# Performance work log

Measured on AMD Instinct MI355X. Metric: run time of the kernel, lower is better.

## Reference

```python
import jax, jax.numpy as jnp
import numpy as np

N = 50000
E = 800000
IN_CH, HID, OUT_CH = 8, 64, 1
NEG_SLOPE = 0.2


def setup_inputs() -> dict:
    key = jax.random.key(0)
    ks = jax.random.split(key, 16)
    x = jax.random.normal(ks[0], (N, IN_CH), dtype=jnp.float32)
    edge_index = jax.random.randint(ks[1], (2, E), 0, N, dtype=jnp.int64)
    def glorot(k, shape):
        fan = shape[0] + shape[-1]
        return jax.random.uniform(k, shape, jnp.float32, -1.0, 1.0) * jnp.sqrt(6.0 / fan)
    # layer 1: in=8 -> 4 heads x 64, concat=False (mean over heads)
    W1 = glorot(ks[2], (IN_CH, 4 * HID))
    as1 = glorot(ks[3], (4, HID)); ad1 = glorot(ks[4], (4, HID))
    b1 = jnp.zeros((HID,), jnp.float32)
    # layer 2: 64 -> 4 heads x 64
    W2 = glorot(ks[5], (HID, 4 * HID))
    as2 = glorot(ks[6], (4, HID)); ad2 = glorot(ks[7], (4, HID))
    b2 = jnp.zeros((HID,), jnp.float32)
    # layer 3: 64 -> 1 head x 1
    W3 = glorot(ks[8], (HID, OUT_CH))
    as3 = glorot(ks[9], (1, OUT_CH)); ad3 = glorot(ks[10], (1, OUT_CH))
    b3 = jnp.zeros((OUT_CH,), jnp.float32)
    return {"x": x, "edge_index": edge_index,
            "W1": W1, "b1": b1, "as1": as1, "ad1": ad1,
            "W2": W2, "b2": b2, "as2": as2, "ad2": ad2,
            "W3": W3, "b3": b3, "as3": as3, "ad3": ad3}


def gat_conv(x, src, dst, W, b, a_src, a_dst, n_nodes):
    """PyG GATConv, concat=False (mean over heads), add_self_loops already applied."""
    heads, ch = a_src.shape
    h = (x @ W).reshape(n_nodes, heads, ch)            # [N,H,C]
    e_src = jnp.sum(h * a_src[None], axis=-1)          # [N,H]
    e_dst = jnp.sum(h * a_dst[None], axis=-1)          # [N,H]
    logits = jax.nn.leaky_relu(e_src[src] + e_dst[dst], NEG_SLOPE)  # [E,H]
    # softmax over incoming edges of each destination node (self loops ensure non-empty)
    m = jax.ops.segment_max(logits, dst, num_segments=n_nodes)      # [N,H]
    ex = jnp.exp(logits - m[dst])
    denom = jax.ops.segment_sum(ex, dst, num_segments=n_nodes)      # [N,H]
    alpha = ex / (denom[dst] + 1e-16)                  # [E,H]
    out = jax.ops.segment_sum(alpha[:, :, None] * h[src], dst, num_segments=n_nodes)  # [N,H,C]
    return jnp.mean(out, axis=1) + b                   # [N,C]


def reference(x, edge_index, W1, b1, as1, ad1, W2, b2, as2, ad2, W3, b3, as3, ad3):
    n = x.shape[0]
    loops = jnp.arange(n, dtype=edge_index.dtype)
    src = jnp.concatenate([edge_index[0], loops])
    dst = jnp.concatenate([edge_index[1], loops])
    h = jax.nn.elu(gat_conv(x, src, dst, W1, b1, as1, ad1, n))
    # Dropout(p=0.2) is identity in eval mode
    h = jax.nn.elu(gat_conv(h, src, dst, W2, b2, as2, ad2, n))
    out = jax.nn.sigmoid(gat_conv(h, src, dst, W3, b3, as3, ad3, n))
    return out  # [N,1] failure probability per node
```

## Files before the change

kernel.cpp:

```cpp
#include <hip/hip_runtime.h>
#include <hip/hip_bf16.h>
#include <hip/hip_fp16.h>
#include <math.h>

#define N_NODES 50000
#define N_EDGES 800000
#define N_TOT   (N_EDGES + N_NODES)
#define NEG_SLOPE 0.2f

static __device__ __forceinline__ float lrelu(float x){ return x >= 0.f ? x : NEG_SLOPE * x; }

__global__ void k_init(const int* __restrict__ ei, int* __restrict__ flag,
                       int* __restrict__ deg){
  int i = blockIdx.x * blockDim.x + threadIdx.x;
  if (i == 0){
    int o = 0;
    #pragma unroll
    for (int j = 1; j < 16; j += 2) o |= ei[j];
    *flag = (o == 0) ? 1 : 0;
  }
  if (i < N_NODES) deg[i] = 1;
}

__global__ void k_count(const int* __restrict__ ei, const int* __restrict__ flag,
                        int* __restrict__ deg){
  int t = blockIdx.x * blockDim.x + threadIdx.x;
  if (t >= N_EDGES / 4) return;
  int d0, d1, d2, d3;
  if (*flag){
    int4 a = *(const int4*)&ei[2 * N_EDGES + 8 * t];
    int4 b = *(const int4*)&ei[2 * N_EDGES + 8 * t + 4];
    d0 = a.x; d1 = a.z; d2 = b.x; d3 = b.z;
  } else {
    int4 a = *(const int4*)&ei[N_EDGES + 4 * t];
    d0 = a.x; d1 = a.y; d2 = a.z; d3 = a.w;
  }
  atomicAdd(&deg[d0], 1);
  atomicAdd(&deg[d1], 1);
  atomicAdd(&deg[d2], 1);
  atomicAdd(&deg[d3], 1);
}

__global__ void k_scan1(const int* __restrict__ deg, int* __restrict__ rowptr,
                        int* __restrict__ bsum){
  __shared__ int sd[256];
  int t = threadIdx.x;
  int base = blockIdx.x * 1024 + t * 4;
  int v0 = (base + 0 < N_NODES) ? deg[base + 0] : 0;
  int v1 = (base + 1 < N_NODES) ? deg[base + 1] : 0;
  int v2 = (base + 2 < N_NODES) ? deg[base + 2] : 0;
  int v3 = (base + 3 < N_NODES) ? deg[base + 3] : 0;
  int tsum = v0 + v1 + v2 + v3;
  sd[t] = tsum; __syncthreads();
  for (int off = 1; off < 256; off <<= 1){
    int vv = (t >= off) ? sd[t - off] : 0;
    __syncthreads();
    sd[t] += vv;
    __syncthreads();
  }
  int excl = sd[t] - tsum;
  if (base + 0 < N_NODES) rowptr[base + 0] = excl;
  if (base + 1 < N_NODES) rowptr[base + 1] = excl + v0;
  if (base + 2 < N_NODES) rowptr[base + 2] = excl + v0 + v1;
  if (base + 3 < N_NODES) rowptr[base + 3] = excl + v0 + v1 + v2;
  if (t == 255) bsum[blockIdx.x] = sd[255];
}

#define NB_SCAN 49
__global__ void k_scan3(int* __restrict__ rowptr, const int* __restrict__ bsum,
                        int* __restrict__ fill){
  __shared__ int sboff[64];
  int t = threadIdx.x;
  if (t < 64){
    int v = (t < NB_SCAN) ? bsum[t] : 0;
    int incl = v;
    #pragma unroll
    for (int off = 1; off < 64; off <<= 1){
      int u = __shfl_up(incl, off);
      if (t >= off) incl += u;
    }
    sboff[t] = incl - v;
  }
  __syncthreads();
  int i = blockIdx.x * blockDim.x + t;
  if (i < N_NODES){
    int v = rowptr[i] + sboff[i >> 10];
    rowptr[i] = v;
    fill[i] = v;
  }
  if (i == 0) rowptr[N_NODES] = N_TOT;
}

__global__ void k_scatter(const int* __restrict__ ei, const int* __restrict__ flag,
                          int* __restrict__ fill, int* __restrict__ col){
  int t = blockIdx.x * blockDim.x + threadIdx.x;
  if (t < N_EDGES / 4){
    int s0, s1, s2, s3, d0, d1, d2, d3;
    if (*flag){
      int4 sa = *(const int4*)&ei[8 * t];
      int4 sb = *(const int4*)&ei[8 * t + 4];
      int4 da = *(const int4*)&ei[2 * N_EDGES + 8 * t];
      int4 db = *(const int4*)&ei[2 * N_EDGES + 8 * t + 4];
      s0 = sa.x; s1 = sa.z; s2 = sb.x; s3 = sb.z;
      d0 = da.x; d1 = da.z; d2 = db.x; d3 = db.z;
    } else {
      int4 sa = *(const int4*)&ei[4 * t];
      int4 da = *(const int4*)&ei[N_EDGES + 4 * t];
      s0 = sa.x; s1 = sa.y; s2 = sa.z; s3 = sa.w;
      d0 = da.x; d1 = da.y; d2 = da.z; d3 = da.w;
    }
    col[atomicAdd(&fill[d0], 1)] = s0;
    col[atomicAdd(&fill[d1], 1)] = s1;
    col[atomicAdd(&fill[d2], 1)] = s2;
    col[atomicAdd(&fill[d3], 1)] = s3;
  } else {
    int n = t - N_EDGES / 4;
    if (n < N_NODES) col[atomicAdd(&fill[n], 1)] = n;
  }
}


__global__ __launch_bounds__(256) void k_transform1(
    const float* __restrict__ xin, const float* __restrict__ W,
    const float* __restrict__ aS, const float* __restrict__ aD,
    __half* __restrict__ h, float* __restrict__ es, float* __restrict__ ed){
  __shared__ float wl[8 * 256];
  int tid = threadIdx.x;
  for (int i = tid; i < 8 * 256; i += 256) wl[i] = W[i];
  int lane = tid & 63, wv = tid >> 6, head = lane >> 4;
  float4 s4 = *(const float4*)&aS[4 * lane];
  float4 d4 = *(const float4*)&aD[4 * lane];
  __syncthreads();
  int base = (blockIdx.x * 4 + wv) * 8;
  for (int m = 0; m < 8; m++){
    int n = base + m;
    if (n >= N_NODES) break;
    float4 xa = *(const float4*)&xin[n * 8];
    float4 xb = *(const float4*)&xin[n * 8 + 4];
    float xs0 = xa.x, xs1 = xa.y, xs2 = xa.z, xs3 = xa.w;
    float xs4 = xb.x, xs5 = xb.y, xs6 = xb.z, xs7 = xb.w;
    float4 acc = make_float4(0.f, 0.f, 0.f, 0.f);
    #define T1STEP(k, xv) { float4 w4 = *(const float4*)&wl[(k)*256 + 4*lane]; \
      acc.x = fmaf(xv, w4.x, acc.x); acc.y = fmaf(xv, w4.y, acc.y); \
      acc.z = fmaf(xv, w4.z, acc.z); acc.w = fmaf(xv, w4.w, acc.w); }
    T1STEP(0, xs0) T1STEP(1, xs1) T1STEP(2, xs2) T1STEP(3, xs3)
    T1STEP(4, xs4) T1STEP(5, xs5) T1STEP(6, xs6) T1STEP(7, xs7)
    #undef T1STEP
    __half2 p0 = __floats2half2_rn(acc.x, acc.y);
    __half2 p1 = __floats2half2_rn(acc.z, acc.w);
    uint2 u; u.x = *(unsigned int*)&p0; u.y = *(unsigned int*)&p1;
    *(uint2*)&h[(size_t)n * 256 + 4 * lane] = u;
    float ps = acc.x*s4.x + acc.y*s4.y + acc.z*s4.z + acc.w*s4.w;
    float pd = acc.x*d4.x + acc.y*d4.y + acc.z*d4.z + acc.w*d4.w;
    #pragma unroll
    for (int off = 1; off < 16; off <<= 1){ ps += __shfl_xor(ps, off); pd += __shfl_xor(pd, off); }
    if ((lane & 15) == 0){ es[n * 4 + head] = ps; ed[n * 4 + head] = pd; }
  }
}

__global__ __launch_bounds__(256) void k_transform2(
    const float* __restrict__ xin, const float* __restrict__ W,
    const float* __restrict__ aS, const float* __restrict__ aD,
    __half* __restrict__ h, float* __restrict__ es, float* __restrict__ ed){
  __shared__ float wl[32 * 256];
  int tid = threadIdx.x;
  int lane = tid & 63, wv = tid >> 6, head = lane >> 4;
  float4 s4 = *(const float4*)&aS[4 * lane];
  float4 d4 = *(const float4*)&aD[4 * lane];
  int base = (blockIdx.x * 4 + wv) * 8;
  float xr[8];
  #pragma unroll
  for (int m = 0; m < 8; m++){
    int n = base + m;
    xr[m] = (n < N_NODES) ? xin[(size_t)n * 64 + lane] : 0.f;
  }
  float4 acc[8];
  #pragma unroll
  for (int m = 0; m < 8; m++) acc[m] = make_float4(0.f, 0.f, 0.f, 0.f);
  for (int hf = 0; hf < 2; hf++){
    if (hf) __syncthreads();
    const float4* Wv = (const float4*)(W + hf * 32 * 256);
    float4* wlv = (float4*)wl;
    #pragma unroll
    for (int i = 0; i < 8; i++) wlv[tid + 256 * i] = Wv[tid + 256 * i];
    __syncthreads();
    #pragma unroll 4
    for (int k = 0; k < 32; k++){
      float4 w4 = *(const float4*)&wl[k * 256 + 4 * lane];
      #pragma unroll
      for (int m = 0; m < 8; m++){
        float xv = __shfl(xr[m], hf * 32 + k);
        acc[m].x = fmaf(xv, w4.x, acc[m].x);
        acc[m].y = fmaf(xv, w4.y, acc[m].y);
        acc[m].z = fmaf(xv, w4.z, acc[m].z);
        acc[m].w = fmaf(xv, w4.w, acc[m].w);
      }
    }
  }
  #pragma unroll
  for (int m = 0; m < 8; m++){
    int n = base + m;
    if (n >= N_NODES) break;
    __half2 p0 = __floats2half2_rn(acc[m].x, acc[m].y);
    __half2 p1 = __floats2half2_rn(acc[m].z, acc[m].w);
    uint2 u; u.x = *(unsigned int*)&p0; u.y = *(unsigned int*)&p1;
    *(uint2*)&h[(size_t)n * 256 + 4 * lane] = u;
    float ps = acc[m].x*s4.x + acc[m].y*s4.y + acc[m].z*s4.z + acc[m].w*s4.w;
    float pd = acc[m].x*d4.x + acc[m].y*d4.y + acc[m].z*d4.z + acc[m].w*d4.w;
    #pragma unroll
    for (int off = 1; off < 16; off <<= 1){ ps += __shfl_xor(ps, off); pd += __shfl_xor(pd, off); }
    if ((lane & 15) == 0){ es[n * 4 + head] = ps; ed[n * 4 + head] = pd; }
  }
}

__global__ __launch_bounds__(256) void k_transform3(
    const float* __restrict__ xin, const float* __restrict__ W3,
    const float* __restrict__ aS, const float* __restrict__ aD,
    float2* __restrict__ pk, float* __restrict__ ed3){
  int gid = blockIdx.x * blockDim.x + threadIdx.x;
  int n = gid >> 6, lane = gid & 63;
  if (n >= N_NODES) return;
  float v = xin[(size_t)n * 64 + lane] * W3[lane];
  #pragma unroll
  for (int off = 1; off < 64; off <<= 1) v += __shfl_xor(v, off);
  if (lane == 0){
    pk[n] = make_float2(v * aS[0], v);
    ed3[n] = v * aD[0];
  }
}

static __device__ __forceinline__ void agg_step(float4& acc, uint2 u, float wt){
  float2 aa = __half22float2(*(__half2*)&u.x);
  float2 bb = __half22float2(*(__half2*)&u.y);
  acc.x = fmaf(wt, aa.x, acc.x); acc.y = fmaf(wt, aa.y, acc.y);
  acc.z = fmaf(wt, bb.x, acc.z); acc.w = fmaf(wt, bb.y, acc.w);
}

__global__ __launch_bounds__(256) void k_agg(
    const __half* __restrict__ h, const float* __restrict__ es, const float* __restrict__ ed,
    const int* __restrict__ rowptr, const int* __restrict__ col,
    const float* __restrict__ bias, float* __restrict__ outf){
  int gid = blockIdx.x * blockDim.x + threadIdx.x;
  int d = gid >> 6, lane = gid & 63;
  if (d >= N_NODES) return;
  int start = rowptr[d], end = rowptr[d + 1];
  int head = lane >> 4;
  float eh = ed[d * 4 + head];
  const __half* hp = h + 4 * lane;
  float4 acc = make_float4(0.f, 0.f, 0.f, 0.f);
  float wsum = 0.f;
  int i = start;
  for (; i + 4 <= end; i += 4){
    int s0 = col[i], s1 = col[i + 1], s2 = col[i + 2], s3 = col[i + 3];
    uint2 u0 = *(const uint2*)(hp + (size_t)s0 * 256);
    uint2 u1 = *(const uint2*)(hp + (size_t)s1 * 256);
    uint2 u2 = *(const uint2*)(hp + (size_t)s2 * 256);
    uint2 u3 = *(const uint2*)(hp + (size_t)s3 * 256);
    float e0 = es[s0 * 4 + head], e1 = es[s1 * 4 + head];
    float e2 = es[s2 * 4 + head], e3 = es[s3 * 4 + head];
    float w0 = __expf(lrelu(e0 + eh));
    float w1 = __expf(lrelu(e1 + eh));
    float w2 = __expf(lrelu(e2 + eh));
    float w3 = __expf(lrelu(e3 + eh));
    wsum += (w0 + w1) + (w2 + w3);
    agg_step(acc, u0, w0); agg_step(acc, u1, w1);
    agg_step(acc, u2, w2); agg_step(acc, u3, w3);
  }
  for (; i < end; i++){
    int s0 = col[i];
    uint2 u0 = *(const uint2*)(hp + (size_t)s0 * 256);
    float w0 = __expf(lrelu(es[s0 * 4 + head] + eh));
    wsum += w0;
    agg_step(acc, u0, w0);
  }
  float inv = 1.0f / (wsum + 1e-16f);
  acc.x *= inv; acc.y *= inv; acc.z *= inv; acc.w *= inv;
  #pragma unroll
  for (int off = 16; off < 64; off <<= 1){
    acc.x += __shfl_xor(acc.x, off);
    acc.y += __shfl_xor(acc.y, off);
    acc.z += __shfl_xor(acc.z, off);
    acc.w += __shfl_xor(acc.w, off);
  }
  if (lane < 16){
    float4 b4 = *(const float4*)&bias[4 * lane];
    float ox = 0.25f * acc.x + b4.x;
    float oy = 0.25f * acc.y + b4.y;
    float oz = 0.25f * acc.z + b4.z;
    float ow = 0.25f * acc.w + b4.w;
    ox = ox > 0.f ? ox : expm1f(ox);
    oy = oy > 0.f ? oy : expm1f(oy);
    oz = oz > 0.f ? oz : expm1f(oz);
    ow = ow > 0.f ? ow : expm1f(ow);
    float4 o = make_float4(ox, oy, oz, ow);
    *(float4*)&outf[(size_t)d * 64 + 4 * lane] = o;
  }
}

__global__ __launch_bounds__(256) void k_agg3(
    const float2* __restrict__ pk, const float* __restrict__ ed3,
    const int* __restrict__ rowptr, const int* __restrict__ col,
    const float* __restrict__ b3, float* __restrict__ out){
  int gid = blockIdx.x * blockDim.x + threadIdx.x;
  int wv = gid >> 6, lane = gid & 63;
  int sub = lane >> 4, li = lane & 15;
  int d = wv * 4 + sub;
  if (d < N_NODES){
    int start = rowptr[d], end = rowptr[d + 1];
    float edv = ed3[d];
    float num = 0.f, den = 0.f;
    for (int i = start + li; i < end; i += 16){
      float2 p = pk[col[i]];
      float wgt = __expf(lrelu(p.x + edv));
      den += wgt;
      num = fmaf(wgt, p.y, num);
    }
    #pragma unroll
    for (int off = 1; off < 16; off <<= 1){
      num += __shfl_xor(num, off);
      den += __shfl_xor(den, off);
    }
    if (li == 0){
      float v = num / (den + 1e-16f) + b3[0];
      out[d] = 1.f / (1.f + __expf(-v));
    }
  }
}

extern "C" void kernel_launch(void* const* d_in, const int* in_sizes, int n_in,
                              void* d_out, int out_size, void* d_ws, size_t ws_size,
                              hipStream_t stream) {
  const float* x   = (const float*)d_in[0];
  const int*   ei  = (const int*)  d_in[1];
  const float* W1  = (const float*)d_in[2];
  const float* b1  = (const float*)d_in[3];
  const float* as1 = (const float*)d_in[4];
  const float* ad1 = (const float*)d_in[5];
  const float* W2  = (const float*)d_in[6];
  const float* b2  = (const float*)d_in[7];
  const float* as2 = (const float*)d_in[8];
  const float* ad2 = (const float*)d_in[9];
  const float* W3  = (const float*)d_in[10];
  const float* b3  = (const float*)d_in[11];
  const float* as3 = (const float*)d_in[12];
  const float* ad3 = (const float*)d_in[13];
  float* out = (float*)d_out;

  char* w = (char*)d_ws;
  size_t off = 0;
  auto alloc = [&](size_t bytes) -> char* {
    char* p = w + off;
    off += (bytes + 255) & ~size_t(255);
    return p;
  };
  int*    flag   = (int*)   alloc(64);
  int*    deg    = (int*)   alloc(N_NODES * 4);
  int*    fill   = (int*)   alloc(N_NODES * 4);
  int*    rowptr = (int*)   alloc((N_NODES + 1) * 4);
  int*    bsum   = (int*)   alloc(64 * 4);
  int*    col    = (int*)   alloc((size_t)N_TOT * 4);
  __half* h      = (__half*)alloc((size_t)N_NODES * 256 * 2);
  float*  es     = (float*) alloc((size_t)N_NODES * 4 * 4);
  float*  ed     = (float*) alloc((size_t)N_NODES * 4 * 4);
  float*  feat1  = (float*) alloc((size_t)N_NODES * 64 * 4);
  float*  feat2  = (float*) alloc((size_t)N_NODES * 64 * 4);
  float2* pk     = (float2*)alloc((size_t)N_NODES * 8);
  float*  ed3    = (float*) alloc(N_NODES * 4);
  (void)ws_size; (void)in_sizes; (void)n_in; (void)out_size;

  k_init   <<<(N_NODES + 255) / 256, 256, 0, stream>>>(ei, flag, deg);
  k_count  <<<(N_EDGES / 4 + 255) / 256, 256, 0, stream>>>(ei, flag, deg);
  k_scan1  <<<NB_SCAN, 256, 0, stream>>>(deg, rowptr, bsum);
  k_scan3  <<<(N_NODES + 255) / 256, 256, 0, stream>>>(rowptr, bsum, fill);
  k_scatter<<<(N_EDGES / 4 + N_NODES + 255) / 256, 256, 0, stream>>>(ei, flag, fill, col);

  const int grid_t12 = (N_NODES + 31) / 32;
  const int grid_wpn = (N_NODES * 64 + 255) / 256;
  const int grid_w4n = ((N_NODES + 3) / 4 * 64 + 255) / 256;

  k_transform1<<<grid_t12, 256, 0, stream>>>(x, W1, as1, ad1, h, es, ed);
  k_agg       <<<grid_wpn, 256, 0, stream>>>(h, es, ed, rowptr, col, b1, feat1);
  k_transform2<<<grid_t12, 256, 0, stream>>>(feat1, W2, as2, ad2, h, es, ed);
  k_agg       <<<grid_wpn, 256, 0, stream>>>(h, es, ed, rowptr, col, b2, feat2);
  k_transform3<<<grid_wpn, 256, 0, stream>>>(feat2, W3, as3, ad3, pk, ed3);
  k_agg3      <<<grid_w4n, 256, 0, stream>>>(pk, ed3, rowptr, col, b3, out);
}
```

Baseline: 394.0 us.

## Fuse CSR count with layer-1 transform and merge scan kernels

Merges degree counting and the layer-1 feature transform into one launch by giving each a separate range of blocks. The two scan passes are collapsed into a single kernel that uses an atomic counter and a spin-wait so each block can read the other blocks' partial sums. The init kernel is replaced by a memset, with the self-loop +1 folded into the scan. Layer-3 transform now packs four nodes per wavefront using float4 loads. The aim is fewer kernel launches and less per-launch overhead, at the cost of a grid-wide spin that relies on all 49 blocks being resident at once.

```diff
diff --git a/kernel.cpp b/kernel.cpp
--- a/kernel.cpp
+++ b/kernel.cpp
@@ -1,5 +1,4 @@
 #include <hip/hip_runtime.h>
-#include <hip/hip_bf16.h>
 #include <hip/hip_fp16.h>
 #include <math.h>
 
@@ -7,49 +6,84 @@
 #define N_EDGES 800000
 #define N_TOT   (N_EDGES + N_NODES)
 #define NEG_SLOPE 0.2f
+#define NB_COUNT 782
+#define NB_SCAN  49
 
 static __device__ __forceinline__ float lrelu(float x){ return x >= 0.f ? x : NEG_SLOPE * x; }
 
-__global__ void k_init(const int* __restrict__ ei, int* __restrict__ flag,
-                       int* __restrict__ deg){
-  int i = blockIdx.x * blockDim.x + threadIdx.x;
-  if (i == 0){
-    int o = 0;
-    #pragma unroll
-    for (int j = 1; j < 16; j += 2) o |= ei[j];
-    *flag = (o == 0) ? 1 : 0;
-  }
-  if (i < N_NODES) deg[i] = 1;
-}
-
-__global__ void k_count(const int* __restrict__ ei, const int* __restrict__ flag,
-                        int* __restrict__ deg){
-  int t = blockIdx.x * blockDim.x + threadIdx.x;
-  if (t >= N_EDGES / 4) return;
-  int d0, d1, d2, d3;
-  if (*flag){
-    int4 a = *(const int4*)&ei[2 * N_EDGES + 8 * t];
-    int4 b = *(const int4*)&ei[2 * N_EDGES + 8 * t + 4];
-    d0 = a.x; d1 = a.z; d2 = b.x; d3 = b.z;
-  } else {
-    int4 a = *(const int4*)&ei[N_EDGES + 4 * t];
-    d0 = a.x; d1 = a.y; d2 = a.z; d3 = a.w;
-  }
-  atomicAdd(&deg[d0], 1);
-  atomicAdd(&deg[d1], 1);
-  atomicAdd(&deg[d2], 1);
-  atomicAdd(&deg[d3], 1);
-}
-
-__global__ void k_scan1(const int* __restrict__ deg, int* __restrict__ rowptr,
-                        int* __restrict__ bsum){
+static __device__ __forceinline__ int edge_flag(const int* __restrict__ ei){
+  int o = 0;
+  #pragma unroll
+  for (int j = 1; j < 16; j += 2) o |= ei[j];
+  return (o == 0) ? 1 : 0;
+}
+
+__global__ __launch_bounds__(256) void kA(
+    const int* __restrict__ ei, int* __restrict__ deg,
+    const float* __restrict__ xin, const float* __restrict__ W,
+    const float* __restrict__ aS, const float* __restrict__ aD,
+    __half* __restrict__ h, float* __restrict__ es, float* __restrict__ ed){
+  __shared__ float wl[8 * 256];
+  if ((int)blockIdx.x < NB_COUNT){
+    int t = blockIdx.x * 256 + threadIdx.x;
+    if (t < N_EDGES / 4){
+      int d0, d1, d2, d3;
+      if (edge_flag(ei)){
+        int4 a = *(const int4*)&ei[2 * N_EDGES + 8 * t];
+        int4 b = *(const int4*)&ei[2 * N_EDGES + 8 * t + 4];
+        d0 = a.x; d1 = a.z; d2 = b.x; d3 = b.z;
+      } else {
+        int4 a = *(const int4*)&ei[N_EDGES + 4 * t];
+        d0 = a.x; d1 = a.y; d2 = a.z; d3 = a.w;
+      }
+      atomicAdd(&deg[d0], 1); atomicAdd(&deg[d1], 1);
+      atomicAdd(&deg[d2], 1); atomicAdd(&deg[d3], 1);
+    }
+    return;
+  }
+  int bid = blockIdx.x - NB_COUNT;
+  int tid = threadIdx.x;
+  for (int i = tid; i < 8 * 256; i += 256) wl[i] = W[i];
+  int lane = tid & 63, wv = tid >> 6, head = lane >> 4;
+  float4 s4 = *(const float4*)&aS[4 * lane];
+  float4 d4 = *(const float4*)&aD[4 * lane];
+  __syncthreads();
+  int base = (bid * 4 + wv) * 8;
+  for (int m = 0; m < 8; m++){
+    int n = base + m;
+    if (n >= N_NODES) break;
+    float4 xa = *(const float4*)&xin[n * 8];
+    float4 xb = *(const float4*)&xin[n * 8 + 4];
+    float4 acc = make_float4(0.f, 0.f, 0.f, 0.f);
+    #define T1STEP(k, xv) { float4 w4 = *(const float4*)&wl[(k)*256 + 4*lane]; \
+      acc.x = fmaf(xv, w4.x, acc.x); acc.y = fmaf(xv, w4.y, acc.y); \
+      acc.z = fmaf(xv, w4.z, acc.z); acc.w = fmaf(xv, w4.w, acc.w); }
+    T1STEP(0, xa.x) T1STEP(1, xa.y) T1STEP(2, xa.z) T1STEP(3, xa.w)
+    T1STEP(4, xb.x) T1STEP(5, xb.y) T1STEP(6, xb.z) T1STEP(7, xb.w)
+    #undef T1STEP
+    __half2 p0 = __floats2half2_rn(acc.x, acc.y);
+    __half2 p1 = __floats2half2_rn(acc.z, acc.w);
+    uint2 u; u.x = *(unsigned int*)&p0; u.y = *(unsigned int*)&p1;
+    *(uint2*)&h[(size_t)n * 256 + 4 * lane] = u;
+    float ps = acc.x*s4.x + acc.y*s4.y + acc.z*s4.z + acc.w*s4.w;
+    float pd = acc.x*d4.x + acc.y*d4.y + acc.z*d4.z + acc.w*d4.w;
+    #pragma unroll
+    for (int off = 1; off < 16; off <<= 1){ ps += __shfl_xor(ps, off); pd += __shfl_xor(pd, off); }
+    if ((lane & 15) == 0){ es[n * 4 + head] = ps; ed[n * 4 + head] = pd; }
+  }
+}
+
+__global__ __launch_bounds__(256) void k_scan(
+    const int* __restrict__ deg, int* __restrict__ rowptr, int* __restrict__ fill,
+    int* __restrict__ bsum, int* __restrict__ done){
   __shared__ int sd[256];
-  int t = threadIdx.x;
-  int base = blockIdx.x * 1024 + t * 4;
-  int v0 = (base + 0 < N_NODES) ? deg[base + 0] : 0;
-  int v1 = (base + 1 < N_NODES) ? deg[base + 1] : 0;
-  int v2 = (base + 2 < N_NODES) ? deg[base + 2] : 0;
-  int v3 = (base + 3 < N_NODES) ? deg[base + 3] : 0;
+  __shared__ int s_off;
+  int b = blockIdx.x, t = threadIdx.x;
+  int base = b * 1024 + t * 4;
+  int v0 = (base + 0 < N_NODES) ? deg[base + 0] + 1 : 0;
+  int v1 = (base + 1 < N_NODES) ? deg[base + 1] + 1 : 0;
+  int v2 = (base + 2 < N_NODES) ? deg[base + 2] + 1 : 0;
+  int v3 = (base + 3 < N_NODES) ? deg[base + 3] + 1 : 0;
   int tsum = v0 + v1 + v2 + v3;
   sd[t] = tsum; __syncthreads();
   for (int off = 1; off < 256; off <<= 1){
@@ -59,44 +93,37 @@
     __syncthreads();
   }
   int excl = sd[t] - tsum;
-  if (base + 0 < N_NODES) rowptr[base + 0] = excl;
-  if (base + 1 < N_NODES) rowptr[base + 1] = excl + v0;
-  if (base + 2 < N_NODES) rowptr[base + 2] = excl + v0 + v1;
-  if (base + 3 < N_NODES) rowptr[base + 3] = excl + v0 + v1 + v2;
-  if (t == 255) bsum[blockIdx.x] = sd[255];
-}
-
-#define NB_SCAN 49
-__global__ void k_scan3(int* __restrict__ rowptr, const int* __restrict__ bsum,
-                        int* __restrict__ fill){
-  __shared__ int sboff[64];
-  int t = threadIdx.x;
+  if (t == 255){
+    atomicExch(&bsum[b], sd[255]);
+    __threadfence();
+    atomicAdd(done, 1);
+  }
+  if (t == 0){
+    while (atomicAdd(done, 0) < NB_SCAN) { }
+  }
+  __syncthreads();
+  __threadfence();
   if (t < 64){
-    int v = (t < NB_SCAN) ? bsum[t] : 0;
-    int incl = v;
-    #pragma unroll
-    for (int off = 1; off < 64; off <<= 1){
-      int u = __shfl_up(incl, off);
-      if (t >= off) incl += u;
-    }
-    sboff[t] = incl - v;
+    int u = (t < b) ? atomicAdd(&bsum[t], 0) : 0;
+    #pragma unroll
+    for (int off = 1; off < 64; off <<= 1) u += __shfl_xor(u, off);
+    if (t == 0) s_off = u;
   }
   __syncthreads();
-  int i = blockIdx.x * blockDim.x + t;
-  if (i < N_NODES){
-    int v = rowptr[i] + sboff[i >> 10];
-    rowptr[i] = v;
-    fill[i] = v;
-  }
-  if (i == 0) rowptr[N_NODES] = N_TOT;
-}
-
-__global__ void k_scatter(const int* __restrict__ ei, const int* __restrict__ flag,
+  int off0 = s_off;
+  if (base + 0 < N_NODES){ int r = excl + off0;                rowptr[base+0] = r; fill[base+0] = r; }
+  if (base + 1 < N_NODES){ int r = excl + v0 + off0;           rowptr[base+1] = r; fill[base+1] = r; }
+  if (base + 2 < N_NODES){ int r = excl + v0 + v1 + off0;      rowptr[base+2] = r; fill[base+2] = r; }
+  if (base + 3 < N_NODES){ int r = excl + v0 + v1 + v2 + off0; rowptr[base+3] = r; fill[base+3] = r; }
+  if (b == 0 && t == 0) rowptr[N_NODES] = N_TOT;
+}
+
+__global__ void k_scatter(const int* __restrict__ ei,
                           int* __restrict__ fill, int* __restrict__ col){
   int t = blockIdx.x * blockDim.x + threadIdx.x;
   if (t < N_EDGES / 4){
     int s0, s1, s2, s3, d0, d1, d2, d3;
-    if (*flag){
+    if (edge_flag(ei)){
       int4 sa = *(const int4*)&ei[8 * t];
       int4 sb = *(const int4*)&ei[8 * t + 4];
       int4 da = *(const int4*)&ei[2 * N_EDGES + 8 * t];
@@ -116,45 +143,6 @@
   } else {
     int n = t - N_EDGES / 4;
     if (n < N_NODES) col[atomicAdd(&fill[n], 1)] = n;
-  }
-}
-
-
-__global__ __launch_bounds__(256) void k_transform1(
-    const float* __restrict__ xin, const float* __restrict__ W,
-    const float* __restrict__ aS, const float* __restrict__ aD,
-    __half* __restrict__ h, float* __restrict__ es, float* __restrict__ ed){
-  __shared__ float wl[8 * 256];
-  int tid = threadIdx.x;
-  for (int i = tid; i < 8 * 256; i += 256) wl[i] = W[i];
-  int lane = tid & 63, wv = tid >> 6, head = lane >> 4;
-  float4 s4 = *(const float4*)&aS[4 * lane];
-  float4 d4 = *(const float4*)&aD[4 * lane];
-  __syncthreads();
-  int base = (blockIdx.x * 4 + wv) * 8;
-  for (int m = 0; m < 8; m++){
-    int n = base + m;
-    if (n >= N_NODES) break;
-    float4 xa = *(const float4*)&xin[n * 8];
-    float4 xb = *(const float4*)&xin[n * 8 + 4];
-    float xs0 = xa.x, xs1 = xa.y, xs2 = xa.z, xs3 = xa.w;
-    float xs4 = xb.x, xs5 = xb.y, xs6 = xb.z, xs7 = xb.w;
-    float4 acc = make_float4(0.f, 0.f, 0.f, 0.f);
-    #define T1STEP(k, xv) { float4 w4 = *(const float4*)&wl[(k)*256 + 4*lane]; \
-      acc.x = fmaf(xv, w4.x, acc.x); acc.y = fmaf(xv, w4.y, acc.y); \
-      acc.z = fmaf(xv, w4.z, acc.z); acc.w = fmaf(xv, w4.w, acc.w); }
-    T1STEP(0, xs0) T1STEP(1, xs1) T1STEP(2, xs2) T1STEP(3, xs3)
-    T1STEP(4, xs4) T1STEP(5, xs5) T1STEP(6, xs6) T1STEP(7, xs7)
-    #undef T1STEP
-    __half2 p0 = __floats2half2_rn(acc.x, acc.y);
-    __half2 p1 = __floats2half2_rn(acc.z, acc.w);
-    uint2 u; u.x = *(unsigned int*)&p0; u.y = *(unsigned int*)&p1;
-    *(uint2*)&h[(size_t)n * 256 + 4 * lane] = u;
-    float ps = acc.x*s4.x + acc.y*s4.y + acc.z*s4.z + acc.w*s4.w;
-    float pd = acc.x*d4.x + acc.y*d4.y + acc.z*d4.z + acc.w*d4.w;
-    #pragma unroll
-    for (int off = 1; off < 16; off <<= 1){ ps += __shfl_xor(ps, off); pd += __shfl_xor(pd, off); }
-    if ((lane & 15) == 0){ es[n * 4 + head] = ps; ed[n * 4 + head] = pd; }
   }
 }
 
@@ -218,14 +206,18 @@
     const float* __restrict__ aS, const float* __restrict__ aD,
     float2* __restrict__ pk, float* __restrict__ ed3){
   int gid = blockIdx.x * blockDim.x + threadIdx.x;
-  int n = gid >> 6, lane = gid & 63;
-  if (n >= N_NODES) return;
-  float v = xin[(size_t)n * 64 + lane] * W3[lane];
-  #pragma unroll
-  for (int off = 1; off < 64; off <<= 1) v += __shfl_xor(v, off);
-  if (lane == 0){
-    pk[n] = make_float2(v * aS[0], v);
-    ed3[n] = v * aD[0];
+  int wv = gid >> 6, lane = gid & 63;
+  int sub = lane >> 4, li = lane & 15;
+  int d = wv * 4 + sub;
+  if (d >= N_NODES) return;
+  float4 xv = *(const float4*)&xin[(size_t)d * 64 + li * 4];
+  float4 w4 = *(const float4*)&W3[li * 4];
+  float v = xv.x*w4.x + xv.y*w4.y + xv.z*w4.z + xv.w*w4.w;
+  #pragma unroll
+  for (int off = 1; off < 16; off <<= 1) v += __shfl_xor(v, off);
+  if (li == 0){
+    pk[d] = make_float2(v * aS[0], v);
+    ed3[d] = v * aD[0];
   }
 }
 
@@ -353,8 +345,8 @@
     off += (bytes + 255) & ~size_t(255);
     return p;
   };
-  int*    flag   = (int*)   alloc(64);
   int*    deg    = (int*)   alloc(N_NODES * 4);
+  int*    done   = (int*)   alloc(256);
   int*    fill   = (int*)   alloc(N_NODES * 4);
   int*    rowptr = (int*)   alloc((N_NODES + 1) * 4);
   int*    bsum   = (int*)   alloc(64 * 4);
@@ -368,20 +360,21 @@
   float*  ed3    = (float*) alloc(N_NODES * 4);
   (void)ws_size; (void)in_sizes; (void)n_in; (void)out_size;
 
-  k_init   <<<(N_NODES + 255) / 256, 256, 0, stream>>>(ei, flag, deg);
-  k_count  <<<(N_EDGES / 4 + 255) / 256, 256, 0, stream>>>(ei, flag, deg);
-  k_scan1  <<<NB_SCAN, 256, 0, stream>>>(deg, rowptr, bsum);
-  k_scan3  <<<(N_NODES + 255) / 256, 256, 0, stream>>>(rowptr, bsum, fill);
-  k_scatter<<<(N_EDGES / 4 + N_NODES + 255) / 256, 256, 0, stream>>>(ei, flag, fill, col);
-
-  const int grid_t12 = (N_NODES + 31) / 32;
+  const size_t degsz = (((size_t)N_NODES * 4 + 255) & ~size_t(255)) + 256;
+  hipMemsetAsync(deg, 0, degsz, stream);
+
+  const int grid_kA  = NB_COUNT + (N_NODES + 31) / 32;
+  const int grid_sct = (N_EDGES / 4 + N_NODES + 255) / 256;
+  const int grid_t2  = (N_NODES + 31) / 32;
   const int grid_wpn = (N_NODES * 64 + 255) / 256;
   const int grid_w4n = ((N_NODES + 3) / 4 * 64 + 255) / 256;
 
-  k_transform1<<<grid_t12, 256, 0, stream>>>(x, W1, as1, ad1, h, es, ed);
-  k_agg       <<<grid_wpn, 256, 0, stream>>>(h, es, ed, rowptr, col, b1, feat1);
-  k_transform2<<<grid_t12, 256, 0, stream>>>(feat1, W2, as2, ad2, h, es, ed);
-  k_agg       <<<grid_wpn, 256, 0, stream>>>(h, es, ed, rowptr, col, b2, feat2);
-  k_transform3<<<grid_wpn, 256, 0, stream>>>(feat2, W3, as3, ad3, pk, ed3);
-  k_agg3      <<<grid_w4n, 256, 0, stream>>>(pk, ed3, rowptr, col, b3, out);
-}
+  kA       <<<grid_kA, 256, 0, stream>>>(ei, deg, x, W1, as1, ad1, h, es, ed);
+  k_scan   <<<NB_SCAN, 256, 0, stream>>>(deg, rowptr, fill, bsum, done);
+  k_scatter<<<grid_sct, 256, 0, stream>>>(ei, fill, col);
+  k_agg    <<<grid_wpn, 256, 0, stream>>>(h, es, ed, rowptr, col, b1, feat1);
+  k_transform2<<<grid_t2, 256, 0, stream>>>(feat1, W2, as2, ad2, h, es, ed);
+  k_agg    <<<grid_wpn, 256, 0, stream>>>(h, es, ed, rowptr, col, b2, feat2);
+  k_transform3<<<grid_w4n, 256, 0, stream>>>(feat2, W3, as3, ad3, pk, ed3);
+  k_agg3   <<<grid_w4n, 256, 0, stream>>>(pk, ed3, rowptr, col, b3, out);
+}
```

Measured after the change: 385.0 us. 2.3% less time.
